# Optimization experiments

Measured on AMD Instinct MI355X. Metric: run time of the kernel, lower is better.

Reference implementation:

```python
import jax, jax.numpy as jnp
import numpy as np

N = 100000   # nodes
E = 1600000  # edges
S = 2000     # subgraphs
G = 64       # graphs
H = 64       # hidden
L = 3        # extra GIN layers after conv1 (num_layers=4)
OUT = 8      # OUTPUT_DIM


def setup_inputs() -> dict:
    key = jax.random.key(0)
    ks = jax.random.split(key, 20)
    s = 0.1
    return {
        "x": jax.random.normal(ks[0], (N, 1), jnp.float32),
        "edge_index": jax.random.randint(ks[1], (2, E), 0, N),
        "node_to_subgraph": jnp.sort(jax.random.randint(ks[2], (N,), 0, S)),
        "subgraph_to_graph": jnp.sort(jax.random.randint(ks[3], (S,), 0, G)),
        # conv1 MLP: Linear(1,H) -> ReLU -> Linear(H,H) -> ReLU
        "conv1_w1": jax.random.normal(ks[4], (1, H), jnp.float32) * s,
        "conv1_b1": jnp.zeros((H,), jnp.float32),
        "conv1_w2": jax.random.normal(ks[5], (H, H), jnp.float32) * s,
        "conv1_b2": jnp.zeros((H,), jnp.float32),
        # remaining L GIN layers, stacked: Linear(H,H) -> ReLU -> Linear(H,H) -> ReLU
        "convs_w1": jax.random.normal(ks[6], (L, H, H), jnp.float32) * s,
        "convs_b1": jnp.zeros((L, H), jnp.float32),
        "convs_w2": jax.random.normal(ks[7], (L, H, H), jnp.float32) * s,
        "convs_b2": jnp.zeros((L, H), jnp.float32),
        "lin1_w": jax.random.normal(ks[8], (H, H), jnp.float32) * s,
        "lin1_b": jnp.zeros((H,), jnp.float32),
        "lin2_w": jax.random.normal(ks[9], (H, OUT), jnp.float32) * s,
        "lin2_b": jnp.zeros((OUT,), jnp.float32),
    }


def _gin_layer(x, src, dst, w1, b1, w2, b2):
    # GINConv with eps=0: mlp(x + sum_{j in N(i)} x_j)
    agg = jax.ops.segment_sum(x[src], dst, num_segments=N)
    h = x + agg
    h = jax.nn.relu(h @ w1 + b1)
    return jax.nn.relu(h @ w2 + b2)


def reference(x, edge_index, node_to_subgraph, subgraph_to_graph,
              conv1_w1, conv1_b1, conv1_w2, conv1_b2,
              convs_w1, convs_b1, convs_w2, convs_b2,
              lin1_w, lin1_b, lin2_w, lin2_b):
    src, dst = edge_index[0], edge_index[1]
    h = _gin_layer(x, src, dst, conv1_w1, conv1_b1, conv1_w2, conv1_b2)
    for i in range(L):
        h = _gin_layer(h, src, dst, convs_w1[i], convs_b1[i], convs_w2[i], convs_b2[i])
    # node -> subgraph -> graph double add-pool
    h = jax.ops.segment_sum(h, node_to_subgraph, num_segments=S)
    h = jax.ops.segment_sum(h, subgraph_to_graph, num_segments=G)
    h = jax.nn.relu(h @ lin1_w + lin1_b)
    h = h @ lin2_w + lin2_b
    return jax.nn.log_softmax(h, axis=-1)
```

## Files before the change

kernel.cpp:

```cpp
#include <hip/hip_runtime.h>
#include <hip/hip_bf16.h>

#define N_NODES 100000
#define N_EDGES 1600000
#define N_SUB   2000
#define N_GRAPH 64
#define HID     64
#define NLAYERS 3
#define SCAN_B  1024
#define N_SCANB ((N_NODES + SCAN_B - 1) / SCAN_B)

__device__ __forceinline__ float bcastf(float v, int l) {
  return __int_as_float(__builtin_amdgcn_readlane(__float_as_int(v), l));
}

__global__ __launch_bounds__(256) void count_slot_kernel(
    const int4* __restrict__ dst4, int* __restrict__ deg,
    int4* __restrict__ slot4) {
  int t = blockIdx.x * blockDim.x + threadIdx.x;
  int nt = gridDim.x * blockDim.x;
  for (int e4 = t; e4 < N_EDGES / 4; e4 += nt) {
    int4 d = dst4[e4];
    int4 p;
    p.x = atomicAdd(&deg[d.x], 1);
    p.y = atomicAdd(&deg[d.y], 1);
    p.z = atomicAdd(&deg[d.z], 1);
    p.w = atomicAdd(&deg[d.w], 1);
    slot4[e4] = p;
  }
}

__global__ __launch_bounds__(SCAN_B) void scan_block_kernel(
    const int* __restrict__ deg, int* __restrict__ rowptr,
    int* __restrict__ partials) {
  __shared__ int sm[SCAN_B];
  const int tid = threadIdx.x;
  const int g = blockIdx.x * SCAN_B + tid;
  int v = (g < N_NODES) ? deg[g] : 0;
  sm[tid] = v;
  __syncthreads();
  for (int off = 1; off < SCAN_B; off <<= 1) {
    int t = (tid >= off) ? sm[tid - off] : 0;
    __syncthreads();
    sm[tid] += t;
    __syncthreads();
  }
  if (g < N_NODES) rowptr[g] = sm[tid] - v;
  if (tid == SCAN_B - 1) partials[blockIdx.x] = sm[tid];
}

__global__ __launch_bounds__(128) void scan_partials_kernel(int* partials) {
  __shared__ int sm[128];
  const int tid = threadIdx.x;
  int v = (tid < N_SCANB) ? partials[tid] : 0;
  sm[tid] = v;
  __syncthreads();
  for (int off = 1; off < 128; off <<= 1) {
    int t = (tid >= off) ? sm[tid - off] : 0;
    __syncthreads();
    sm[tid] += t;
    __syncthreads();
  }
  if (tid < N_SCANB) partials[tid] = sm[tid] - v;
}

__global__ __launch_bounds__(SCAN_B) void add_offsets_kernel(
    int* __restrict__ rowptr, const int* __restrict__ partials) {
  const int g = blockIdx.x * SCAN_B + threadIdx.x;
  if (g < N_NODES) rowptr[g] += partials[blockIdx.x];
  if (g == 0) rowptr[N_NODES] = N_EDGES;
}

__global__ __launch_bounds__(256) void fill_csr2_kernel(
    const int4* __restrict__ src4, const int4* __restrict__ dst4,
    const int4* __restrict__ slot4, const int* __restrict__ rowptr,
    int* __restrict__ csr) {
  int t = blockIdx.x * blockDim.x + threadIdx.x;
  int nt = gridDim.x * blockDim.x;
  for (int e4 = t; e4 < N_EDGES / 4; e4 += nt) {
    int4 s = src4[e4];
    int4 d = dst4[e4];
    int4 p = slot4[e4];
    csr[rowptr[d.x] + p.x] = s.x;
    csr[rowptr[d.y] + p.y] = s.y;
    csr[rowptr[d.z] + p.z] = s.z;
    csr[rowptr[d.w] + p.w] = s.w;
  }
}

__global__ __launch_bounds__(256) void conv1_agg_kernel(
    const float* __restrict__ x, const int* __restrict__ rowptr,
    const int* __restrict__ csr, float* __restrict__ agg1) {
  int t = blockIdx.x * blockDim.x + threadIdx.x;
  int nt = gridDim.x * blockDim.x;
  for (int i = t; i < N_NODES; i += nt) {
    float a = x[i];
    int end = rowptr[i + 1];
    for (int e = rowptr[i]; e < end; e++) a += x[csr[e]];
    agg1[i] = a;
  }
}

__global__ __launch_bounds__(256) void conv1_mlp(
    const float* __restrict__ agg1,
    const float* __restrict__ w1, const float* __restrict__ b1,
    const float* __restrict__ w2, const float* __restrict__ b2,
    float* __restrict__ h) {
  const int lane = threadIdx.x & 63;
  const int wid = (blockIdx.x * blockDim.x + threadIdx.x) >> 6;
  const int nw = (gridDim.x * blockDim.x) >> 6;
  const float w1l = w1[lane], b1l = b1[lane], b2l = b2[lane];
  float w2c[64];
#pragma unroll
  for (int k = 0; k < 64; k++) w2c[k] = w2[k * 64 + lane];

  for (int i = wid; i < N_NODES; i += nw) {
    float hv = agg1[i];
    float y1 = fmaxf(hv * w1l + b1l, 0.f);
    float a0 = b2l, a1 = 0.f, a2 = 0.f, a3 = 0.f;
#pragma unroll
    for (int k = 0; k < 64; k += 4) {
      a0 += bcastf(y1, k)     * w2c[k];
      a1 += bcastf(y1, k + 1) * w2c[k + 1];
      a2 += bcastf(y1, k + 2) * w2c[k + 2];
      a3 += bcastf(y1, k + 3) * w2c[k + 3];
    }
    h[i * 64 + lane] = fmaxf(a0 + a1 + a2 + a3, 0.f);
  }
}

__global__ __launch_bounds__(256) void gather64_f4_kernel(
    const float4* __restrict__ h4, const int* __restrict__ rowptr,
    const int* __restrict__ csr, float4* __restrict__ agg4) {
  const int lane = threadIdx.x & 63;
  const int q = lane >> 4;
  const int sub = lane & 15;
  const int wid = (blockIdx.x * blockDim.x + threadIdx.x) >> 6;
  const int nw = (gridDim.x * blockDim.x) >> 6;
  for (int i = wid; i < N_NODES; i += nw) {
    const int beg = rowptr[i], end = rowptr[i + 1];
    float ax = 0.f, ay = 0.f, az = 0.f, aw = 0.f;
    for (int c = beg; c < end; c += 64) {
      const int nb = min(64, end - c);
      int idx = csr[c + min(lane, nb - 1)];
      for (int j = 0; j < nb; j += 4) {
        int li = j + q;
        int s = __shfl(idx, li < nb ? li : 0, 64);
        float4 v = h4[(size_t)s * 16 + sub];
        if (li < nb) { ax += v.x; ay += v.y; az += v.z; aw += v.w; }
      }
    }
    ax += __shfl_xor(ax, 16, 64); ay += __shfl_xor(ay, 16, 64);
    az += __shfl_xor(az, 16, 64); aw += __shfl_xor(aw, 16, 64);
    ax += __shfl_xor(ax, 32, 64); ay += __shfl_xor(ay, 32, 64);
    az += __shfl_xor(az, 32, 64); aw += __shfl_xor(aw, 32, 64);
    if (q == 0) {
      float4 self = h4[(size_t)i * 16 + sub];
      float4 r;
      r.x = ax + self.x; r.y = ay + self.y;
      r.z = az + self.z; r.w = aw + self.w;
      agg4[(size_t)i * 16 + sub] = r;
    }
  }
}

__global__ __launch_bounds__(256) void gin_mlp(
    const float* __restrict__ agg,
    const float* __restrict__ w1, const float* __restrict__ b1,
    const float* __restrict__ w2, const float* __restrict__ b2,
    float* __restrict__ h) {
  const int lane = threadIdx.x & 63;
  const int wid = (blockIdx.x * blockDim.x + threadIdx.x) >> 6;
  const int nw = (gridDim.x * blockDim.x) >> 6;
  const float b1l = b1[lane], b2l = b2[lane];
  float w1c[64], w2c[64];
#pragma unroll
  for (int k = 0; k < 64; k++) {
    w1c[k] = w1[k * 64 + lane];
    w2c[k] = w2[k * 64 + lane];
  }

  for (int i = wid; i < N_NODES; i += nw) {
    float in = agg[i * 64 + lane];
    float a0 = b1l, a1 = 0.f, a2 = 0.f, a3 = 0.f;
#pragma unroll
    for (int k = 0; k < 64; k += 4) {
      a0 += bcastf(in, k)     * w1c[k];
      a1 += bcastf(in, k + 1) * w1c[k + 1];
      a2 += bcastf(in, k + 2) * w1c[k + 2];
      a3 += bcastf(in, k + 3) * w1c[k + 3];
    }
    float y1 = fmaxf(a0 + a1 + a2 + a3, 0.f);
    a0 = b2l; a1 = 0.f; a2 = 0.f; a3 = 0.f;
#pragma unroll
    for (int k = 0; k < 64; k += 4) {
      a0 += bcastf(y1, k)     * w2c[k];
      a1 += bcastf(y1, k + 1) * w2c[k + 1];
      a2 += bcastf(y1, k + 2) * w2c[k + 2];
      a3 += bcastf(y1, k + 3) * w2c[k + 3];
    }
    h[i * 64 + lane] = fmaxf(a0 + a1 + a2 + a3, 0.f);
  }
}

__global__ __launch_bounds__(256) void pool_nodes(
    const float* __restrict__ h, const int* __restrict__ n2s,
    float* __restrict__ sub) {
  const int lane = threadIdx.x & 63;
  const int wid = (blockIdx.x * blockDim.x + threadIdx.x) >> 6;
  const int nw = (gridDim.x * blockDim.x) >> 6;
  for (int i = wid; i < N_NODES; i += nw) {
    int s = n2s[i];
    atomicAdd(&sub[s * 64 + lane], h[i * 64 + lane]);
  }
}

__global__ __launch_bounds__(256) void pool_sub(
    const float* __restrict__ sub, const int* __restrict__ s2g,
    float* __restrict__ gp) {
  const int lane = threadIdx.x & 63;
  const int wid = (blockIdx.x * blockDim.x + threadIdx.x) >> 6;
  const int nw = (gridDim.x * blockDim.x) >> 6;
  for (int s = wid; s < N_SUB; s += nw) {
    int g = s2g[s];
    atomicAdd(&gp[g * 64 + lane], sub[s * 64 + lane]);
  }
}

__global__ __launch_bounds__(64) void head_kernel(
    const float* __restrict__ gp,
    const float* __restrict__ w1, const float* __restrict__ b1,
    const float* __restrict__ w2, const float* __restrict__ b2,
    float* __restrict__ out) {
  const int g = blockIdx.x;
  const int lane = threadIdx.x;
  float v = gp[g * 64 + lane];
  float acc = b1[lane];
#pragma unroll
  for (int k = 0; k < 64; k++) acc += bcastf(v, k) * w1[k * 64 + lane];
  float y1 = fmaxf(acc, 0.f);
  const int o = lane & 7;
  float acc2 = b2[o];
#pragma unroll
  for (int k = 0; k < 64; k++) acc2 += bcastf(y1, k) * w2[k * 8 + o];
  float m = -1e30f;
#pragma unroll
  for (int oo = 0; oo < 8; oo++) m = fmaxf(m, bcastf(acc2, oo));
  float s = 0.f;
#pragma unroll
  for (int oo = 0; oo < 8; oo++) s += expf(bcastf(acc2, oo) - m);
  float ls = logf(s);
  if (lane < 8) out[g * 8 + lane] = acc2 - m - ls;
}

extern "C" void kernel_launch(void* const* d_in, const int* in_sizes, int n_in,
                              void* d_out, int out_size, void* d_ws,
                              size_t ws_size, hipStream_t stream) {
  const float* x   = (const float*)d_in[0];
  const int* ei    = (const int*)d_in[1];
  const int* src   = ei;
  const int* dst   = ei + N_EDGES;
  const int* n2s   = (const int*)d_in[2];
  const int* s2g   = (const int*)d_in[3];
  const float* c1w1 = (const float*)d_in[4];
  const float* c1b1 = (const float*)d_in[5];
  const float* c1w2 = (const float*)d_in[6];
  const float* c1b2 = (const float*)d_in[7];
  const float* cw1  = (const float*)d_in[8];
  const float* cb1  = (const float*)d_in[9];
  const float* cw2  = (const float*)d_in[10];
  const float* cb2  = (const float*)d_in[11];
  const float* l1w  = (const float*)d_in[12];
  const float* l1b  = (const float*)d_in[13];
  const float* l2w  = (const float*)d_in[14];
  const float* l2b  = (const float*)d_in[15];

  char* p = (char*)d_ws;
  float* h      = (float*)p;  p += (size_t)N_NODES * 64 * 4;
  float* agg    = (float*)p;  p += (size_t)N_NODES * 64 * 4;
  int*   csr    = (int*)p;    p += (size_t)N_EDGES * 4;
  int*   rowptr = (int*)p;    p += (size_t)(N_NODES + 1) * 4;
  int*   deg    = (int*)p;    p += (size_t)N_NODES * 4;
  int*   part   = (int*)p;    p += 256 * 4;
  float* agg1   = (float*)p;  p += (size_t)N_NODES * 4;
  float* sub    = (float*)p;  p += (size_t)N_SUB * 64 * 4;
  float* gp     = (float*)p;  p += (size_t)N_GRAPH * 64 * 4;
  if ((size_t)(p - (char*)d_ws) > ws_size) return;

  int* slot = (int*)agg;

  float* outf = (float*)d_out;

  hipMemsetAsync(deg, 0, N_NODES * sizeof(int), stream);
  count_slot_kernel<<<2048, 256, 0, stream>>>(
      (const int4*)dst, deg, (int4*)slot);
  scan_block_kernel<<<N_SCANB, SCAN_B, 0, stream>>>(deg, rowptr, part);
  scan_partials_kernel<<<1, 128, 0, stream>>>(part);
  add_offsets_kernel<<<N_SCANB, SCAN_B, 0, stream>>>(rowptr, part);
  fill_csr2_kernel<<<2048, 256, 0, stream>>>(
      (const int4*)src, (const int4*)dst, (const int4*)slot, rowptr, csr);

  conv1_agg_kernel<<<1024, 256, 0, stream>>>(x, rowptr, csr, agg1);
  conv1_mlp<<<1024, 256, 0, stream>>>(agg1, c1w1, c1b1, c1w2, c1b2, h);

  for (int l = 0; l < NLAYERS; l++) {
    gather64_f4_kernel<<<2048, 256, 0, stream>>>(
        (const float4*)h, rowptr, csr, (float4*)agg);
    gin_mlp<<<1024, 256, 0, stream>>>(agg, cw1 + l * 64 * 64, cb1 + l * 64,
                                      cw2 + l * 64 * 64, cb2 + l * 64, h);
  }

  hipMemsetAsync(sub, 0, N_SUB * 64 * sizeof(float), stream);
  hipMemsetAsync(gp, 0, N_GRAPH * 64 * sizeof(float), stream);
  pool_nodes<<<1024, 256, 0, stream>>>(h, n2s, sub);
  pool_sub<<<64, 256, 0, stream>>>(sub, s2g, gp);
  head_kernel<<<N_GRAPH, 64, 0, stream>>>(gp, l1w, l1b, l2w, l2b, outf);
}
```

Baseline: 608.4 us.

## Build CSR with per-block private histograms and unroll neighbor gather by four

Replaces the global degree atomics and stored per-edge slot array with 64 per-block private histograms over node ids. A column-wise scan then turns these into per-block offsets and degrees, and the fill kernel takes slots with atomics on the block-private histogram, which should cut contention on hot counters. The gather kernel also issues four neighbor row loads per iteration to raise memory-level parallelism. The cost is a 25.6 MB histogram memset plus scan traffic, and only 64 blocks for the count and fill passes, which may underuse the GPU.

```diff
diff --git a/kernel.cpp b/kernel.cpp
--- a/kernel.cpp
+++ b/kernel.cpp
@@ -9,25 +9,38 @@
 #define NLAYERS 3
 #define SCAN_B  1024
 #define N_SCANB ((N_NODES + SCAN_B - 1) / SCAN_B)
+#define NB      64
+#define E4_PER_B (N_EDGES / 4 / NB)
 
 __device__ __forceinline__ float bcastf(float v, int l) {
   return __int_as_float(__builtin_amdgcn_readlane(__float_as_int(v), l));
 }
 
-__global__ __launch_bounds__(256) void count_slot_kernel(
-    const int4* __restrict__ dst4, int* __restrict__ deg,
-    int4* __restrict__ slot4) {
-  int t = blockIdx.x * blockDim.x + threadIdx.x;
-  int nt = gridDim.x * blockDim.x;
-  for (int e4 = t; e4 < N_EDGES / 4; e4 += nt) {
-    int4 d = dst4[e4];
-    int4 p;
-    p.x = atomicAdd(&deg[d.x], 1);
-    p.y = atomicAdd(&deg[d.y], 1);
-    p.z = atomicAdd(&deg[d.z], 1);
-    p.w = atomicAdd(&deg[d.w], 1);
-    slot4[e4] = p;
-  }
+__global__ __launch_bounds__(1024) void hist_count_kernel(
+    const int4* __restrict__ dst4, int* __restrict__ hist) {
+  const int b = blockIdx.x;
+  int* my = hist + (size_t)b * N_NODES;
+  for (int t = threadIdx.x; t < E4_PER_B; t += 1024) {
+    int4 d = dst4[b * E4_PER_B + t];
+    atomicAdd(&my[d.x], 1);
+    atomicAdd(&my[d.y], 1);
+    atomicAdd(&my[d.z], 1);
+    atomicAdd(&my[d.w], 1);
+  }
+}
+
+__global__ __launch_bounds__(256) void hist_scan_kernel(
+    int* __restrict__ hist, int* __restrict__ deg) {
+  const int i = blockIdx.x * 256 + threadIdx.x;
+  if (i >= N_NODES) return;
+  int run = 0;
+#pragma unroll
+  for (int b = 0; b < NB; b++) {
+    int v = hist[(size_t)b * N_NODES + i];
+    hist[(size_t)b * N_NODES + i] = run;
+    run += v;
+  }
+  deg[i] = run;
 }
 
 __global__ __launch_bounds__(SCAN_B) void scan_block_kernel(
@@ -71,20 +84,24 @@
   if (g == 0) rowptr[N_NODES] = N_EDGES;
 }
 
-__global__ __launch_bounds__(256) void fill_csr2_kernel(
+__global__ __launch_bounds__(1024) void fill_csr3_kernel(
     const int4* __restrict__ src4, const int4* __restrict__ dst4,
-    const int4* __restrict__ slot4, const int* __restrict__ rowptr,
+    const int* __restrict__ rowptr, int* __restrict__ hist,
     int* __restrict__ csr) {
-  int t = blockIdx.x * blockDim.x + threadIdx.x;
-  int nt = gridDim.x * blockDim.x;
-  for (int e4 = t; e4 < N_EDGES / 4; e4 += nt) {
+  const int b = blockIdx.x;
+  int* my = hist + (size_t)b * N_NODES;
+  for (int t = threadIdx.x; t < E4_PER_B; t += 1024) {
+    int e4 = b * E4_PER_B + t;
     int4 s = src4[e4];
     int4 d = dst4[e4];
-    int4 p = slot4[e4];
-    csr[rowptr[d.x] + p.x] = s.x;
-    csr[rowptr[d.y] + p.y] = s.y;
-    csr[rowptr[d.z] + p.z] = s.z;
-    csr[rowptr[d.w] + p.w] = s.w;
+    int px = atomicAdd(&my[d.x], 1);
+    int py = atomicAdd(&my[d.y], 1);
+    int pz = atomicAdd(&my[d.z], 1);
+    int pw = atomicAdd(&my[d.w], 1);
+    csr[rowptr[d.x] + px] = s.x;
+    csr[rowptr[d.y] + py] = s.y;
+    csr[rowptr[d.z] + pz] = s.z;
+    csr[rowptr[d.w] + pw] = s.w;
   }
 }
 
@@ -143,7 +160,22 @@
     for (int c = beg; c < end; c += 64) {
       const int nb = min(64, end - c);
       int idx = csr[c + min(lane, nb - 1)];
-      for (int j = 0; j < nb; j += 4) {
+      int j = 0;
+      for (; j + 16 <= nb; j += 16) {
+        int s0 = __shfl(idx, j + q, 64);
+        int s1 = __shfl(idx, j + 4 + q, 64);
+        int s2 = __shfl(idx, j + 8 + q, 64);
+        int s3 = __shfl(idx, j + 12 + q, 64);
+        float4 v0 = h4[(size_t)s0 * 16 + sub];
+        float4 v1 = h4[(size_t)s1 * 16 + sub];
+        float4 v2 = h4[(size_t)s2 * 16 + sub];
+        float4 v3 = h4[(size_t)s3 * 16 + sub];
+        ax += (v0.x + v1.x) + (v2.x + v3.x);
+        ay += (v0.y + v1.y) + (v2.y + v3.y);
+        az += (v0.z + v1.z) + (v2.z + v3.z);
+        aw += (v0.w + v1.w) + (v2.w + v3.w);
+      }
+      for (; j < nb; j += 4) {
         int li = j + q;
         int s = __shfl(idx, li < nb ? li : 0, 64);
         float4 v = h4[(size_t)s * 16 + sub];
@@ -287,18 +319,18 @@
   float* gp     = (float*)p;  p += (size_t)N_GRAPH * 64 * 4;
   if ((size_t)(p - (char*)d_ws) > ws_size) return;
 
-  int* slot = (int*)agg;
+  int* hist = (int*)agg;
 
   float* outf = (float*)d_out;
 
-  hipMemsetAsync(deg, 0, N_NODES * sizeof(int), stream);
-  count_slot_kernel<<<2048, 256, 0, stream>>>(
-      (const int4*)dst, deg, (int4*)slot);
+  hipMemsetAsync(hist, 0, (size_t)NB * N_NODES * sizeof(int), stream);
+  hist_count_kernel<<<NB, 1024, 0, stream>>>((const int4*)dst, hist);
+  hist_scan_kernel<<<(N_NODES + 255) / 256, 256, 0, stream>>>(hist, deg);
   scan_block_kernel<<<N_SCANB, SCAN_B, 0, stream>>>(deg, rowptr, part);
   scan_partials_kernel<<<1, 128, 0, stream>>>(part);
   add_offsets_kernel<<<N_SCANB, SCAN_B, 0, stream>>>(rowptr, part);
-  fill_csr2_kernel<<<2048, 256, 0, stream>>>(
-      (const int4*)src, (const int4*)dst, (const int4*)slot, rowptr, csr);
+  fill_csr3_kernel<<<NB, 1024, 0, stream>>>(
+      (const int4*)src, (const int4*)dst, rowptr, hist, csr);
 
   conv1_agg_kernel<<<1024, 256, 0, stream>>>(x, rowptr, csr, agg1);
   conv1_mlp<<<1024, 256, 0, stream>>>(agg1, c1w1, c1b1, c1w2, c1b2, h);
```

Measured after the change: 695.6 us. 14.3% more time.

## Slice degree histogram, unroll neighbor gather, fuse last GIN MLP with node pooling

Applied to the files above, without the earlier changes.

The degree-count atomics are spread across 8 per-block-slice histograms, and a new per-node pass scans those slices to produce degree totals and per-slice offsets. The CSR fill adds the slice offset, which cuts contention on the same address for high-degree nodes. The gather inner loop is unrolled to issue four float4 loads per step for more memory-level parallelism. The last layer's MLP now atomically adds its output straight into the subgraph pool, so the h write/read and a separate pool kernel are dropped, at the cost of one extra small kernel and a larger memset for the histograms.

```diff
diff --git a/kernel.cpp b/kernel.cpp
--- a/kernel.cpp
+++ b/kernel.cpp
@@ -9,25 +9,42 @@
 #define NLAYERS 3
 #define SCAN_B  1024
 #define N_SCANB ((N_NODES + SCAN_B - 1) / SCAN_B)
+#define NSLICE  8
+#define FILL_GRID 2048
 
 __device__ __forceinline__ float bcastf(float v, int l) {
   return __int_as_float(__builtin_amdgcn_readlane(__float_as_int(v), l));
 }
 
-__global__ __launch_bounds__(256) void count_slot_kernel(
-    const int4* __restrict__ dst4, int* __restrict__ deg,
+__global__ __launch_bounds__(256) void count_slot8_kernel(
+    const int4* __restrict__ dst4, int* __restrict__ hist8,
     int4* __restrict__ slot4) {
   int t = blockIdx.x * blockDim.x + threadIdx.x;
   int nt = gridDim.x * blockDim.x;
+  int* my = hist8 + (size_t)(blockIdx.x & (NSLICE - 1)) * N_NODES;
   for (int e4 = t; e4 < N_EDGES / 4; e4 += nt) {
     int4 d = dst4[e4];
     int4 p;
-    p.x = atomicAdd(&deg[d.x], 1);
-    p.y = atomicAdd(&deg[d.y], 1);
-    p.z = atomicAdd(&deg[d.z], 1);
-    p.w = atomicAdd(&deg[d.w], 1);
+    p.x = atomicAdd(&my[d.x], 1);
+    p.y = atomicAdd(&my[d.y], 1);
+    p.z = atomicAdd(&my[d.z], 1);
+    p.w = atomicAdd(&my[d.w], 1);
     slot4[e4] = p;
   }
+}
+
+__global__ __launch_bounds__(256) void hist_scan8_kernel(
+    int* __restrict__ hist8, int* __restrict__ deg) {
+  const int i = blockIdx.x * 256 + threadIdx.x;
+  if (i >= N_NODES) return;
+  int run = 0;
+#pragma unroll
+  for (int s = 0; s < NSLICE; s++) {
+    int v = hist8[(size_t)s * N_NODES + i];
+    hist8[(size_t)s * N_NODES + i] = run;
+    run += v;
+  }
+  deg[i] = run;
 }
 
 __global__ __launch_bounds__(SCAN_B) void scan_block_kernel(
@@ -71,20 +88,21 @@
   if (g == 0) rowptr[N_NODES] = N_EDGES;
 }
 
-__global__ __launch_bounds__(256) void fill_csr2_kernel(
+__global__ __launch_bounds__(256) void fill_csr4_kernel(
     const int4* __restrict__ src4, const int4* __restrict__ dst4,
     const int4* __restrict__ slot4, const int* __restrict__ rowptr,
-    int* __restrict__ csr) {
+    const int* __restrict__ hist8, int* __restrict__ csr) {
   int t = blockIdx.x * blockDim.x + threadIdx.x;
   int nt = gridDim.x * blockDim.x;
+  const int* my = hist8 + (size_t)(blockIdx.x & (NSLICE - 1)) * N_NODES;
   for (int e4 = t; e4 < N_EDGES / 4; e4 += nt) {
     int4 s = src4[e4];
     int4 d = dst4[e4];
     int4 p = slot4[e4];
-    csr[rowptr[d.x] + p.x] = s.x;
-    csr[rowptr[d.y] + p.y] = s.y;
-    csr[rowptr[d.z] + p.z] = s.z;
-    csr[rowptr[d.w] + p.w] = s.w;
+    csr[rowptr[d.x] + my[d.x] + p.x] = s.x;
+    csr[rowptr[d.y] + my[d.y] + p.y] = s.y;
+    csr[rowptr[d.z] + my[d.z] + p.z] = s.z;
+    csr[rowptr[d.w] + my[d.w] + p.w] = s.w;
   }
 }
 
@@ -143,7 +161,22 @@
     for (int c = beg; c < end; c += 64) {
       const int nb = min(64, end - c);
       int idx = csr[c + min(lane, nb - 1)];
-      for (int j = 0; j < nb; j += 4) {
+      int j = 0;
+      for (; j + 16 <= nb; j += 16) {
+        int s0 = __shfl(idx, j + q, 64);
+        int s1 = __shfl(idx, j + 4 + q, 64);
+        int s2 = __shfl(idx, j + 8 + q, 64);
+        int s3 = __shfl(idx, j + 12 + q, 64);
+        float4 v0 = h4[(size_t)s0 * 16 + sub];
+        float4 v1 = h4[(size_t)s1 * 16 + sub];
+        float4 v2 = h4[(size_t)s2 * 16 + sub];
+        float4 v3 = h4[(size_t)s3 * 16 + sub];
+        ax += (v0.x + v1.x) + (v2.x + v3.x);
+        ay += (v0.y + v1.y) + (v2.y + v3.y);
+        az += (v0.z + v1.z) + (v2.z + v3.z);
+        aw += (v0.w + v1.w) + (v2.w + v3.w);
+      }
+      for (; j < nb; j += 4) {
         int li = j + q;
         int s = __shfl(idx, li < nb ? li : 0, 64);
         float4 v = h4[(size_t)s * 16 + sub];
@@ -203,15 +236,43 @@
   }
 }
 
-__global__ __launch_bounds__(256) void pool_nodes(
-    const float* __restrict__ h, const int* __restrict__ n2s,
-    float* __restrict__ sub) {
-  const int lane = threadIdx.x & 63;
-  const int wid = (blockIdx.x * blockDim.x + threadIdx.x) >> 6;
-  const int nw = (gridDim.x * blockDim.x) >> 6;
+__global__ __launch_bounds__(256) void gin_mlp_pool(
+    const float* __restrict__ agg,
+    const float* __restrict__ w1, const float* __restrict__ b1,
+    const float* __restrict__ w2, const float* __restrict__ b2,
+    const int* __restrict__ n2s, float* __restrict__ sub) {
+  const int lane = threadIdx.x & 63;
+  const int wid = (blockIdx.x * blockDim.x + threadIdx.x) >> 6;
+  const int nw = (gridDim.x * blockDim.x) >> 6;
+  const float b1l = b1[lane], b2l = b2[lane];
+  float w1c[64], w2c[64];
+#pragma unroll
+  for (int k = 0; k < 64; k++) {
+    w1c[k] = w1[k * 64 + lane];
+    w2c[k] = w2[k * 64 + lane];
+  }
+
   for (int i = wid; i < N_NODES; i += nw) {
-    int s = n2s[i];
-    atomicAdd(&sub[s * 64 + lane], h[i * 64 + lane]);
+    float in = agg[i * 64 + lane];
+    float a0 = b1l, a1 = 0.f, a2 = 0.f, a3 = 0.f;
+#pragma unroll
+    for (int k = 0; k < 64; k += 4) {
+      a0 += bcastf(in, k)     * w1c[k];
+      a1 += bcastf(in, k + 1) * w1c[k + 1];
+      a2 += bcastf(in, k + 2) * w1c[k + 2];
+      a3 += bcastf(in, k + 3) * w1c[k + 3];
+    }
+    float y1 = fmaxf(a0 + a1 + a2 + a3, 0.f);
+    a0 = b2l; a1 = 0.f; a2 = 0.f; a3 = 0.f;
+#pragma unroll
+    for (int k = 0; k < 64; k += 4) {
+      a0 += bcastf(y1, k)     * w2c[k];
+      a1 += bcastf(y1, k + 1) * w2c[k + 1];
+      a2 += bcastf(y1, k + 2) * w2c[k + 2];
+      a3 += bcastf(y1, k + 3) * w2c[k + 3];
+    }
+    float y2 = fmaxf(a0 + a1 + a2 + a3, 0.f);
+    atomicAdd(&sub[(size_t)n2s[i] * 64 + lane], y2);
   }
 }
 
@@ -287,32 +348,41 @@
   float* gp     = (float*)p;  p += (size_t)N_GRAPH * 64 * 4;
   if ((size_t)(p - (char*)d_ws) > ws_size) return;
 
-  int* slot = (int*)agg;
+  int* hist8 = (int*)agg;
+  int* slot  = (int*)agg + (size_t)NSLICE * N_NODES;
 
   float* outf = (float*)d_out;
 
-  hipMemsetAsync(deg, 0, N_NODES * sizeof(int), stream);
-  count_slot_kernel<<<2048, 256, 0, stream>>>(
-      (const int4*)dst, deg, (int4*)slot);
+  hipMemsetAsync(hist8, 0, (size_t)NSLICE * N_NODES * sizeof(int), stream);
+  count_slot8_kernel<<<FILL_GRID, 256, 0, stream>>>(
+      (const int4*)dst, hist8, (int4*)slot);
+  hist_scan8_kernel<<<(N_NODES + 255) / 256, 256, 0, stream>>>(hist8, deg);
   scan_block_kernel<<<N_SCANB, SCAN_B, 0, stream>>>(deg, rowptr, part);
   scan_partials_kernel<<<1, 128, 0, stream>>>(part);
   add_offsets_kernel<<<N_SCANB, SCAN_B, 0, stream>>>(rowptr, part);
-  fill_csr2_kernel<<<2048, 256, 0, stream>>>(
-      (const int4*)src, (const int4*)dst, (const int4*)slot, rowptr, csr);
+  fill_csr4_kernel<<<FILL_GRID, 256, 0, stream>>>(
+      (const int4*)src, (const int4*)dst, (const int4*)slot, rowptr, hist8,
+      csr);
 
   conv1_agg_kernel<<<1024, 256, 0, stream>>>(x, rowptr, csr, agg1);
   conv1_mlp<<<1024, 256, 0, stream>>>(agg1, c1w1, c1b1, c1w2, c1b2, h);
+
+  hipMemsetAsync(sub, 0, N_SUB * 64 * sizeof(float), stream);
+  hipMemsetAsync(gp, 0, N_GRAPH * 64 * sizeof(float), stream);
 
   for (int l = 0; l < NLAYERS; l++) {
     gather64_f4_kernel<<<2048, 256, 0, stream>>>(
         (const float4*)h, rowptr, csr, (float4*)agg);
-    gin_mlp<<<1024, 256, 0, stream>>>(agg, cw1 + l * 64 * 64, cb1 + l * 64,
-                                      cw2 + l * 64 * 64, cb2 + l * 64, h);
-  }
-
-  hipMemsetAsync(sub, 0, N_SUB * 64 * sizeof(float), stream);
-  hipMemsetAsync(gp, 0, N_GRAPH * 64 * sizeof(float), stream);
-  pool_nodes<<<1024, 256, 0, stream>>>(h, n2s, sub);
+    if (l < NLAYERS - 1) {
+      gin_mlp<<<1024, 256, 0, stream>>>(agg, cw1 + l * 64 * 64, cb1 + l * 64,
+                                        cw2 + l * 64 * 64, cb2 + l * 64, h);
+    } else {
+      gin_mlp_pool<<<1024, 256, 0, stream>>>(
+          agg, cw1 + l * 64 * 64, cb1 + l * 64, cw2 + l * 64 * 64,
+          cb2 + l * 64, n2s, sub);
+    }
+  }
+
   pool_sub<<<64, 256, 0, stream>>>(sub, s2g, gp);
   head_kernel<<<N_GRAPH, 64, 0, stream>>>(gp, l1w, l1b, l2w, l2b, outf);
 }
```

Result: faster. 592.4 us (-2.6%).

## Unroll gather loop, fuse last GIN MLP with node pooling, widen MLP grids

Applied to the files above, without the earlier changes.

The neighbor gather loop is unrolled by four so each lane issues four independent float4 loads per iteration, with a masked tail loop for leftovers. The last GIN layer's MLP now atomically adds its output straight into the subgraph pool. This removes the final write of h and the separate pool_nodes pass over it. The MLP kernels also launch with 2048 blocks instead of 1024, which changes occupancy but keeps the per-thread weight register arrays.

```diff
diff --git a/kernel.cpp b/kernel.cpp
--- a/kernel.cpp
+++ b/kernel.cpp
@@ -143,7 +143,22 @@
     for (int c = beg; c < end; c += 64) {
       const int nb = min(64, end - c);
       int idx = csr[c + min(lane, nb - 1)];
-      for (int j = 0; j < nb; j += 4) {
+      int j = 0;
+      for (; j + 16 <= nb; j += 16) {
+        int s0 = __shfl(idx, j + q, 64);
+        int s1 = __shfl(idx, j + 4 + q, 64);
+        int s2 = __shfl(idx, j + 8 + q, 64);
+        int s3 = __shfl(idx, j + 12 + q, 64);
+        float4 v0 = h4[(size_t)s0 * 16 + sub];
+        float4 v1 = h4[(size_t)s1 * 16 + sub];
+        float4 v2 = h4[(size_t)s2 * 16 + sub];
+        float4 v3 = h4[(size_t)s3 * 16 + sub];
+        ax += (v0.x + v1.x) + (v2.x + v3.x);
+        ay += (v0.y + v1.y) + (v2.y + v3.y);
+        az += (v0.z + v1.z) + (v2.z + v3.z);
+        aw += (v0.w + v1.w) + (v2.w + v3.w);
+      }
+      for (; j < nb; j += 4) {
         int li = j + q;
         int s = __shfl(idx, li < nb ? li : 0, 64);
         float4 v = h4[(size_t)s * 16 + sub];
@@ -203,15 +218,43 @@
   }
 }
 
-__global__ __launch_bounds__(256) void pool_nodes(
-    const float* __restrict__ h, const int* __restrict__ n2s,
-    float* __restrict__ sub) {
-  const int lane = threadIdx.x & 63;
-  const int wid = (blockIdx.x * blockDim.x + threadIdx.x) >> 6;
-  const int nw = (gridDim.x * blockDim.x) >> 6;
+__global__ __launch_bounds__(256) void gin_mlp_pool(
+    const float* __restrict__ agg,
+    const float* __restrict__ w1, const float* __restrict__ b1,
+    const float* __restrict__ w2, const float* __restrict__ b2,
+    const int* __restrict__ n2s, float* __restrict__ sub) {
+  const int lane = threadIdx.x & 63;
+  const int wid = (blockIdx.x * blockDim.x + threadIdx.x) >> 6;
+  const int nw = (gridDim.x * blockDim.x) >> 6;
+  const float b1l = b1[lane], b2l = b2[lane];
+  float w1c[64], w2c[64];
+#pragma unroll
+  for (int k = 0; k < 64; k++) {
+    w1c[k] = w1[k * 64 + lane];
+    w2c[k] = w2[k * 64 + lane];
+  }
+
   for (int i = wid; i < N_NODES; i += nw) {
-    int s = n2s[i];
-    atomicAdd(&sub[s * 64 + lane], h[i * 64 + lane]);
+    float in = agg[i * 64 + lane];
+    float a0 = b1l, a1 = 0.f, a2 = 0.f, a3 = 0.f;
+#pragma unroll
+    for (int k = 0; k < 64; k += 4) {
+      a0 += bcastf(in, k)     * w1c[k];
+      a1 += bcastf(in, k + 1) * w1c[k + 1];
+      a2 += bcastf(in, k + 2) * w1c[k + 2];
+      a3 += bcastf(in, k + 3) * w1c[k + 3];
+    }
+    float y1 = fmaxf(a0 + a1 + a2 + a3, 0.f);
+    a0 = b2l; a1 = 0.f; a2 = 0.f; a3 = 0.f;
+#pragma unroll
+    for (int k = 0; k < 64; k += 4) {
+      a0 += bcastf(y1, k)     * w2c[k];
+      a1 += bcastf(y1, k + 1) * w2c[k + 1];
+      a2 += bcastf(y1, k + 2) * w2c[k + 2];
+      a3 += bcastf(y1, k + 3) * w2c[k + 3];
+    }
+    float y2 = fmaxf(a0 + a1 + a2 + a3, 0.f);
+    atomicAdd(&sub[(size_t)n2s[i] * 64 + lane], y2);
   }
 }
 
@@ -301,18 +344,25 @@
       (const int4*)src, (const int4*)dst, (const int4*)slot, rowptr, csr);
 
   conv1_agg_kernel<<<1024, 256, 0, stream>>>(x, rowptr, csr, agg1);
-  conv1_mlp<<<1024, 256, 0, stream>>>(agg1, c1w1, c1b1, c1w2, c1b2, h);
-
-  for (int l = 0; l < NLAYERS; l++) {
-    gather64_f4_kernel<<<2048, 256, 0, stream>>>(
-        (const float4*)h, rowptr, csr, (float4*)agg);
-    gin_mlp<<<1024, 256, 0, stream>>>(agg, cw1 + l * 64 * 64, cb1 + l * 64,
-                                      cw2 + l * 64 * 64, cb2 + l * 64, h);
-  }
+  conv1_mlp<<<2048, 256, 0, stream>>>(agg1, c1w1, c1b1, c1w2, c1b2, h);
 
   hipMemsetAsync(sub, 0, N_SUB * 64 * sizeof(float), stream);
   hipMemsetAsync(gp, 0, N_GRAPH * 64 * sizeof(float), stream);
-  pool_nodes<<<1024, 256, 0, stream>>>(h, n2s, sub);
+
+  gather64_f4_kernel<<<2048, 256, 0, stream>>>(
+      (const float4*)h, rowptr, csr, (float4*)agg);
+  gin_mlp<<<2048, 256, 0, stream>>>(agg, cw1 + 0 * 4096, cb1 + 0 * 64,
+                                    cw2 + 0 * 4096, cb2 + 0 * 64, h);
+  gather64_f4_kernel<<<2048, 256, 0, stream>>>(
+      (const float4*)h, rowptr, csr, (float4*)agg);
+  gin_mlp<<<2048, 256, 0, stream>>>(agg, cw1 + 1 * 4096, cb1 + 1 * 64,
+                                    cw2 + 1 * 4096, cb2 + 1 * 64, h);
+  gather64_f4_kernel<<<2048, 256, 0, stream>>>(
+      (const float4*)h, rowptr, csr, (float4*)agg);
+  gin_mlp_pool<<<2048, 256, 0, stream>>>(agg, cw1 + 2 * 4096, cb1 + 2 * 64,
+                                         cw2 + 2 * 4096, cb2 + 2 * 64,
+                                         n2s, sub);
+
   pool_sub<<<64, 256, 0, stream>>>(sub, s2g, gp);
   head_kernel<<<N_GRAPH, 64, 0, stream>>>(gp, l1w, l1b, l2w, l2b, outf);
 }
```

Measured after the change: 583.0 us. 4.2% less time.
